# Performance work log

Hardware: AMD Instinct MI355X
Metric: run time of the kernel (lower is better)

The kernel has to match this reference:

```python
import jax, jax.numpy as jnp
import numpy as np

L = 19                      # blur kernel side
K2 = L * L                  # 361 taps
PAD1 = L // 2               # 9 (left/top)
PAD2 = L // 2               # 9 (right/bottom, l odd)


def _sv_blur(x, kernel):
    """Spatially-varying blur: out[b,c,i,j] = sum_k patch_k(x)[b,c,i,j]*kernel[b,k,i,j] / K2.

    Divisor: the torch module always recomputes divisor = fold(unfold(ones)).sum(1)
    (padded size H+18 != 128 init size), and with fold kernel_size=1 this is the
    constant L*L everywhere.
    """
    B, C, H, W = x.shape
    pad = jnp.pad(x, ((0, 0), (0, 0), (PAD1, PAD2), (PAD1, PAD2)), mode='reflect')
    # Extract LxL patches per pixel; single-channel batch of B*C maps, so output
    # channel ordering is row-major over (u, v) kernel offsets, matching torch unfold.
    xr = pad.reshape(B * C, 1, H + PAD1 + PAD2, W + PAD1 + PAD2)
    patches = jax.lax.conv_general_dilated_patches(
        xr, filter_shape=(L, L), window_strides=(1, 1), padding='VALID')  # [B*C, K2, H, W]
    patches = patches.reshape(B, C, K2, H, W)
    out = jnp.einsum('bckhw,bkhw->bchw', patches, kernel)
    return out / jnp.asarray(K2, dtype=out.dtype)


def setup_inputs() -> dict:
    key = jax.random.key(0)
    k1, k2 = jax.random.split(key)
    B, C, H, W = 2, 3, 256, 256
    inp = jax.random.normal(k1, (B, C, H, W), dtype=jnp.float32)
    kernel = jax.random.uniform(k2, (B, K2, H, W), dtype=jnp.float32)
    return {"input": inp, "kernel": kernel}


def reference(input, kernel):
    return _sv_blur(input, kernel)
```

## Files before the change

### kernel.cpp

```cpp
#include <hip/hip_runtime.h>


#define LW     19
#define PAD    9
#define K2     361
#define HH     256
#define WW     256
#define CC     3
#define TILE_W 64
#define TILE_H 4
#define SM_W   (TILE_W + LW - 1)
#define SM_H   (TILE_H + LW - 1)

__global__ __launch_bounds__(256)
void svblur_kernel(const float* __restrict__ x,
                   const float* __restrict__ ker,
                   float* __restrict__ out) {
    __shared__ float tile[CC][SM_H][SM_W];

    const int tx  = threadIdx.x;
    const int ty  = threadIdx.y;
    const int tid = ty * TILE_W + tx;
    const int j0  = blockIdx.x * TILE_W;
    const int i0  = blockIdx.y * TILE_H;
    const int b   = blockIdx.z;

    const float* xb = x + (size_t)b * CC * HH * WW;
    for (int idx = tid; idx < CC * SM_H * SM_W; idx += 256) {
        int c  = idx / (SM_H * SM_W);
        int rm = idx - c * (SM_H * SM_W);
        int r  = rm / SM_W;
        int cc = rm - r * SM_W;
        int gr = i0 + r - PAD;
        gr = gr < 0 ? -gr : (gr >= HH ? 2 * HH - 2 - gr : gr);
        int gc = j0 + cc - PAD;
        gc = gc < 0 ? -gc : (gc >= WW ? 2 * WW - 2 - gc : gc);
        ((float*)tile)[idx] = xb[((size_t)c * HH + gr) * WW + gc];
    }
    __syncthreads();

    const int i = i0 + ty;
    const int j = j0 + tx;
    const float* kp = ker + ((size_t)b * K2 * HH + i) * WW + j;

    float a0 = 0.f, a1 = 0.f, a2 = 0.f;
    for (int u = 0; u < LW; ++u) {
        const float* r0 = &tile[0][ty + u][tx];
        const float* r1 = &tile[1][ty + u][tx];
        const float* r2 = &tile[2][ty + u][tx];
        const float* kq = kp + (size_t)(u * LW) * (HH * WW);
        #pragma unroll
        for (int v = 0; v < LW; ++v) {
            float kv = kq[(size_t)v * (HH * WW)];
            a0 = fmaf(r0[v], kv, a0);
            a1 = fmaf(r1[v], kv, a1);
            a2 = fmaf(r2[v], kv, a2);
        }
    }

    const float s = 1.0f / (float)K2;
    float* op = out + (((size_t)b * CC) * HH + i) * WW + j;
    op[0 * (HH * WW)] = a0 * s;
    op[1 * (HH * WW)] = a1 * s;
    op[2 * (HH * WW)] = a2 * s;
}

extern "C" void kernel_launch(void* const* d_in, const int* in_sizes, int n_in,
                              void* d_out, int out_size, void* d_ws, size_t ws_size,
                              hipStream_t stream) {
    const float* x   = (const float*)d_in[0];
    const float* ker = (const float*)d_in[1];
    float* out       = (float*)d_out;

    dim3 grid(WW / TILE_W, HH / TILE_H, 2);
    dim3 block(TILE_W, TILE_H, 1);
    svblur_kernel<<<grid, block, 0, stream>>>(x, ker, out);
}
```

Measured before the change: 263.5 us.

## Process two pixels per thread with float2 loads and register double-buffered kernel prefetch

Each thread now computes two adjacent output pixels, loading kernel weights as float2 and reading the shared tile as float2 windows held in registers. Kernel-weight rows are prefetched into two alternating register buffers, and the first row is fetched before the shared tile is filled so global latency overlaps the tile load and the FMAs. The aim is to cut global and shared load instruction counts and hide memory latency on what is a bandwidth-bound stream of 361 weight planes. In exchange, register pressure goes up sharply (two 19-entry float2 buffers plus windows), which may lower occupancy, and the grid has half as many blocks.

```diff
diff --git a/kernel.cpp b/kernel.cpp
--- a/kernel.cpp
+++ b/kernel.cpp
@@ -7,10 +7,40 @@
 #define HH     256
 #define WW     256
 #define CC     3
-#define TILE_W 64
-#define TILE_H 4
+#define HW     (HH * WW)
+#define TPX    2
+#define TX     64
+#define TY     4
+#define TILE_W (TX * TPX)
+#define TILE_H TY
 #define SM_W   (TILE_W + LW - 1)
 #define SM_H   (TILE_H + LW - 1)
+
+#define PREFETCH_ROW(u_, buf_)                                              \
+  {                                                                         \
+    _Pragma("unroll")                                                       \
+    for (int v = 0; v < LW; ++v)                                            \
+      (buf_)[v] = *(const float2*)(kp + (size_t)((u_) * LW + v) * HW);      \
+  }
+
+#define COMPUTE_ROW(u_, buf_)                                               \
+  {                                                                         \
+    _Pragma("unroll")                                                       \
+    for (int c = 0; c < CC; ++c) {                                          \
+      const float* wp = &tile[c][ty + (u_)][tx * TPX];                      \
+      float2 w[10];                                                         \
+      _Pragma("unroll")                                                     \
+      for (int q = 0; q < 10; ++q) w[q] = *(const float2*)(wp + q * 2);     \
+      _Pragma("unroll")                                                     \
+      for (int v = 0; v < LW; ++v) {                                        \
+        const float xe = ((v) & 1) ? w[(v) >> 1].y : w[(v) >> 1].x;         \
+        const float xo = (((v) + 1) & 1) ? w[((v) + 1) >> 1].y              \
+                                         : w[((v) + 1) >> 1].x;             \
+        acc[c].x = fmaf(xe, (buf_)[v].x, acc[c].x);                         \
+        acc[c].y = fmaf(xo, (buf_)[v].y, acc[c].y);                         \
+      }                                                                     \
+    }                                                                       \
+  }
 
 __global__ __launch_bounds__(256)
 void svblur_kernel(const float* __restrict__ x,
@@ -20,13 +50,20 @@
 
     const int tx  = threadIdx.x;
     const int ty  = threadIdx.y;
-    const int tid = ty * TILE_W + tx;
+    const int tid = ty * TX + tx;
     const int j0  = blockIdx.x * TILE_W;
     const int i0  = blockIdx.y * TILE_H;
     const int b   = blockIdx.z;
 
-    const float* xb = x + (size_t)b * CC * HH * WW;
-    for (int idx = tid; idx < CC * SM_H * SM_W; idx += 256) {
+    const int i  = i0 + ty;
+    const int jj = j0 + tx * TPX;
+    const float* kp = ker + ((size_t)b * K2 * HH + i) * WW + jj;
+
+    float2 bufA[LW], bufB[LW];
+    PREFETCH_ROW(0, bufA);
+
+    const float* xb = x + (size_t)b * CC * HW;
+    for (int idx = tid; idx < CC * SM_H * SM_W; idx += TX * TY) {
         int c  = idx / (SM_H * SM_W);
         int rm = idx - c * (SM_H * SM_W);
         int r  = rm / SM_W;
@@ -39,30 +76,26 @@
     }
     __syncthreads();
 
-    const int i = i0 + ty;
-    const int j = j0 + tx;
-    const float* kp = ker + ((size_t)b * K2 * HH + i) * WW + j;
+    float2 acc[CC] = {};
 
-    float a0 = 0.f, a1 = 0.f, a2 = 0.f;
-    for (int u = 0; u < LW; ++u) {
-        const float* r0 = &tile[0][ty + u][tx];
-        const float* r1 = &tile[1][ty + u][tx];
-        const float* r2 = &tile[2][ty + u][tx];
-        const float* kq = kp + (size_t)(u * LW) * (HH * WW);
-        #pragma unroll
-        for (int v = 0; v < LW; ++v) {
-            float kv = kq[(size_t)v * (HH * WW)];
-            a0 = fmaf(r0[v], kv, a0);
-            a1 = fmaf(r1[v], kv, a1);
-            a2 = fmaf(r2[v], kv, a2);
-        }
+    #pragma unroll
+    for (int u = 0; u < LW - 1; u += 2) {
+        PREFETCH_ROW(u + 1, bufB);
+        COMPUTE_ROW(u, bufA);
+        PREFETCH_ROW(u + 2, bufA);
+        COMPUTE_ROW(u + 1, bufB);
     }
+    COMPUTE_ROW(LW - 1, bufA);
 
     const float s = 1.0f / (float)K2;
-    float* op = out + (((size_t)b * CC) * HH + i) * WW + j;
-    op[0 * (HH * WW)] = a0 * s;
-    op[1 * (HH * WW)] = a1 * s;
-    op[2 * (HH * WW)] = a2 * s;
+    float* op = out + (((size_t)b * CC) * HH + i) * WW + jj;
+    #pragma unroll
+    for (int c = 0; c < CC; ++c) {
+        float2 r;
+        r.x = acc[c].x * s;
+        r.y = acc[c].y * s;
+        *(float2*)(op + (size_t)c * HW) = r;
+    }
 }
 
 extern "C" void kernel_launch(void* const* d_in, const int* in_sizes, int n_in,
@@ -73,6 +106,6 @@
     float* out       = (float*)d_out;
 
     dim3 grid(WW / TILE_W, HH / TILE_H, 2);
-    dim3 block(TILE_W, TILE_H, 1);
+    dim3 block(TX, TY, 1);
     svblur_kernel<<<grid, block, 0, stream>>>(x, ker, out);
 }
```

New measurement: 264.7 us. No clear change (+0.5%).
